# Kernel tuning notes

Measured on AMD Instinct MI355X. Metric: run time of the kernel, lower is better.

## Reference

```python
import jax, jax.numpy as jnp
import numpy as np

N_NODES = 50000
N_EDGES = 600000
IC, H, OC = 64, 128, 32
EPS = 1e-5


def setup_inputs() -> dict:
    key = jax.random.key(0)
    ks = jax.random.split(key, 8)
    x = jax.random.normal(ks[0], (N_NODES, IC), dtype=jnp.float32)
    ei = jax.random.randint(ks[1], (2, N_EDGES), 0, N_NODES, dtype=jnp.int64)
    proj_w = jax.random.normal(ks[2], (IC, H), dtype=jnp.float32) * 0.05
    proj_b = jnp.zeros((H,), dtype=jnp.float32)
    # conv_w[layer, lin, :, :] with lin order: key, query, value, skip
    conv_w = jax.random.normal(ks[3], (3, 4, H, H), dtype=jnp.float32) * 0.05
    conv_b = jnp.zeros((3, 4, H), dtype=jnp.float32)
    bn_gamma = jnp.ones((3, H), dtype=jnp.float32)
    bn_beta = jnp.zeros((3, H), dtype=jnp.float32)
    head_w = jax.random.normal(ks[4], (H, OC), dtype=jnp.float32) * 0.05
    head_b = jnp.zeros((OC,), dtype=jnp.float32)
    return {"x": x, "ei": ei, "proj_w": proj_w, "proj_b": proj_b,
            "conv_w": conv_w, "conv_b": conv_b, "bn_gamma": bn_gamma,
            "bn_beta": bn_beta, "head_w": head_w, "head_b": head_b}


def _res_gated_conv(x, src, dst, w, b):
    # PyG ResGatedGraphConv: out_i = skip(x_i) + sum_j sigmoid(key(x_i)+query(x_j)) * value(x_j)
    k = x @ w[0] + b[0]      # key   (applied to target/dst)
    q = x @ w[1] + b[1]      # query (applied to source/src)
    v = x @ w[2] + b[2]      # value (applied to source/src)
    msg = jax.nn.sigmoid(k[dst] + q[src]) * v[src]          # [E, H]
    agg = jax.ops.segment_sum(msg, dst, num_segments=x.shape[0])  # [N, H]
    return x @ w[3] + b[3] + agg


def _batchnorm(x, gamma, beta):
    # training-mode BatchNorm1d: batch statistics over the node dimension
    mean = jnp.mean(x, axis=0)
    var = jnp.var(x, axis=0)
    return gamma * (x - mean) * jax.lax.rsqrt(var + EPS) + beta


def reference(x, ei, proj_w, proj_b, conv_w, conv_b, bn_gamma, bn_beta, head_w, head_b):
    src, dst = ei[0], ei[1]
    h = jax.nn.relu(x @ proj_w + proj_b)
    for layer in range(3):
        h = _res_gated_conv(h, src, dst, conv_w[layer], conv_b[layer])
        h = jax.nn.relu(_batchnorm(h, bn_gamma[layer], bn_beta[layer]))
        # dropout(p=0.2) is identity in eval mode
    return h @ head_w + head_b
```

## Files before the change

kernel.cpp:

```cpp
#include <hip/hip_runtime.h>
#include <hip/hip_bf16.h>
#include <math.h>

#define HDIM 128
#define ICDIM 64
#define OCDIM 32
#define BN_EPS 1e-5f
#define NCH 64

typedef __attribute__((ext_vector_type(8))) short bv8;
typedef __attribute__((ext_vector_type(4))) float fv4;

static __device__ __forceinline__ unsigned short f2bf(float v) {
    __hip_bfloat16 t = __float2bfloat16(v);
    return *(unsigned short*)&t;
}
static __device__ __forceinline__ float bflo(unsigned int u) {
    union { unsigned int i; float f; } c; c.i = u << 16; return c.f;
}
static __device__ __forceinline__ float bfhi(unsigned int u) {
    union { unsigned int i; float f; } c; c.i = u & 0xffff0000u; return c.f;
}

__global__ void proj_kernel(const float* __restrict__ x,
                            const float* __restrict__ w,
                            const float* __restrict__ b,
                            __hip_bfloat16* __restrict__ h, int n) {
    __shared__ float xs[2][ICDIM];
    int tid = threadIdx.x;
    if (tid < 2 * ICDIM) {
        int r = tid / ICDIM, c = tid % ICDIM;
        int node = blockIdx.x * 2 + r;
        xs[r][c] = (node < n) ? x[(size_t)node * ICDIM + c] : 0.f;
    }
    __syncthreads();
    int node = blockIdx.x * 2 + (tid >> 7);
    if (node >= n) return;
    int c = tid & 127;
    const float* xr = xs[tid >> 7];
    float acc = b[c];
#pragma unroll
    for (int k = 0; k < ICDIM; ++k)
        acc = fmaf(xr[k], w[k * HDIM + c], acc);
    h[(size_t)node * HDIM + c] = __float2bfloat16(fmaxf(acc, 0.f));
}

__global__ void wconv_kernel(const float* __restrict__ src,
                             __hip_bfloat16* __restrict__ dst) {
    int mat = blockIdx.x;
    const float* s = src + (size_t)mat * HDIM * HDIM;
    __hip_bfloat16* d = dst + (size_t)mat * HDIM * HDIM;
    for (int idx = threadIdx.x; idx < HDIM * HDIM; idx += 256) {
        int i = idx >> 7, o = idx & 127;
        d[(size_t)o * HDIM + i] = __float2bfloat16(s[idx]);
    }
}

__global__ __launch_bounds__(1024)
void gemm4_fused_kernel(const __hip_bfloat16* __restrict__ hB,
                        const __hip_bfloat16* __restrict__ wt4,
                        const float* __restrict__ b4,
                        __hip_bfloat16* __restrict__ K,
                        __hip_bfloat16* __restrict__ Q,
                        __hip_bfloat16* __restrict__ V,
                        float* __restrict__ S, int n) {
    __shared__ unsigned short hs[NCH * HDIM];
    const unsigned short* h = (const unsigned short*)hB;
    int tid = threadIdx.x;
    int m0 = blockIdx.x * NCH;

    {
        const uint4* src = (const uint4*)(h + (size_t)m0 * HDIM);
        ((uint4*)hs)[tid] = src[tid];
    }

    int wv = tid >> 6;
    int lane = tid & 63;
    int lin = wv >> 2;
    int g2 = wv & 3;
    int j = lane & 15;
    int kg = lane >> 4;

    const unsigned short* wbase =
        (const unsigned short*)(wt4 + (size_t)lin * HDIM * HDIM);
    bv8 af[2][4];
#pragma unroll
    for (int gs = 0; gs < 2; ++gs)
#pragma unroll
        for (int ks = 0; ks < 4; ++ks)
            af[gs][ks] = *(const bv8*)(wbase +
                (size_t)(g2 * 32 + gs * 16 + j) * HDIM + ks * 32 + kg * 8);

    const float* bl = b4 + lin * HDIM;
    float4 bias0 = *(const float4*)(bl + g2 * 32 + kg * 4);
    float4 bias1 = *(const float4*)(bl + g2 * 32 + 16 + kg * 4);

    __hip_bfloat16* obf = (lin == 0) ? K : (lin == 1) ? Q : V;

    __syncthreads();

#pragma unroll
    for (int t4 = 0; t4 < NCH / 16; ++t4) {
        const unsigned short* hrow = hs + (t4 * 16 + j) * HDIM + kg * 8;
        fv4 acc0 = (fv4){0.f, 0.f, 0.f, 0.f};
        fv4 acc1 = (fv4){0.f, 0.f, 0.f, 0.f};
#pragma unroll
        for (int ks = 0; ks < 4; ++ks) {
            bv8 bf = *(const bv8*)(hrow + ks * 32);
            acc0 = __builtin_amdgcn_mfma_f32_16x16x32_bf16(af[0][ks], bf, acc0, 0, 0, 0);
            acc1 = __builtin_amdgcn_mfma_f32_16x16x32_bf16(af[1][ks], bf, acc1, 0, 0, 0);
        }
        int node = m0 + t4 * 16 + j;
        if (node < n) {
            if (lin == 3) {
                float* o = S + (size_t)node * HDIM + g2 * 32 + kg * 4;
                float4 r0, r1;
                r0.x = acc0.x + bias0.x; r0.y = acc0.y + bias0.y;
                r0.z = acc0.z + bias0.z; r0.w = acc0.w + bias0.w;
                r1.x = acc1.x + bias1.x; r1.y = acc1.y + bias1.y;
                r1.z = acc1.z + bias1.z; r1.w = acc1.w + bias1.w;
                *(float4*)o = r0;
                *(float4*)(o + 16) = r1;
            } else {
                unsigned short* o =
                    (unsigned short*)obf + (size_t)node * HDIM + g2 * 32 + kg * 4;
                ushort4 r0, r1;
                r0.x = f2bf(acc0.x + bias0.x); r0.y = f2bf(acc0.y + bias0.y);
                r0.z = f2bf(acc0.z + bias0.z); r0.w = f2bf(acc0.w + bias0.w);
                r1.x = f2bf(acc1.x + bias1.x); r1.y = f2bf(acc1.y + bias1.y);
                r1.z = f2bf(acc1.z + bias1.z); r1.w = f2bf(acc1.w + bias1.w);
                *(ushort4*)o = r0;
                *(ushort4*)(o + 16) = r1;
            }
        }
    }
}

__global__ void hist_kernel(const int* __restrict__ ei, int* __restrict__ deg, int e) {
    int i = blockIdx.x * 256 + threadIdx.x;
    if (i < e) atomicAdd(&deg[ei[(size_t)e + i]], 1);
}

__global__ void scan1_kernel(const int* __restrict__ deg, int* __restrict__ incl,
                             int* __restrict__ bsum, int n) {
    __shared__ int tmp[256];
    int i = blockIdx.x * 256 + threadIdx.x;
    int v = (i < n) ? deg[i] : 0;
    tmp[threadIdx.x] = v;
    __syncthreads();
    for (int ofs = 1; ofs < 256; ofs <<= 1) {
        int t = (threadIdx.x >= ofs) ? tmp[threadIdx.x - ofs] : 0;
        __syncthreads();
        tmp[threadIdx.x] += t;
        __syncthreads();
    }
    if (i < n) incl[i] = tmp[threadIdx.x];
    if (threadIdx.x == 255) bsum[blockIdx.x] = tmp[255];
}

__global__ void scan2_kernel(int* __restrict__ bsum, int nb) {
    __shared__ int tmp[256];
    int v = (threadIdx.x < nb) ? bsum[threadIdx.x] : 0;
    tmp[threadIdx.x] = v;
    __syncthreads();
    for (int ofs = 1; ofs < 256; ofs <<= 1) {
        int t = (threadIdx.x >= ofs) ? tmp[threadIdx.x - ofs] : 0;
        __syncthreads();
        tmp[threadIdx.x] += t;
        __syncthreads();
    }
    if (threadIdx.x < nb) bsum[threadIdx.x] = tmp[threadIdx.x] - v;
}

__global__ void scan3_kernel(const int* __restrict__ deg, const int* __restrict__ incl,
                             const int* __restrict__ bsum, int* __restrict__ off,
                             int* __restrict__ cursor, int n, int e) {
    int i = blockIdx.x * 256 + threadIdx.x;
    if (i < n) {
        int ex = incl[i] - deg[i] + bsum[blockIdx.x];
        off[i] = ex;
        cursor[i] = ex;
        if (i == n - 1) off[n] = e;
    }
}

__global__ void scatter_kernel(const int* __restrict__ ei, int* __restrict__ cursor,
                               int* __restrict__ esrc, int e) {
    int i = blockIdx.x * 256 + threadIdx.x;
    if (i < e) {
        int dst = ei[(size_t)e + i];
        int pos = atomicAdd(&cursor[dst], 1);
        esrc[pos] = ei[i];
    }
}

__global__ void agg_kernel(const int* __restrict__ off, const int* __restrict__ esrc,
                           const __hip_bfloat16* __restrict__ kb,
                           const __hip_bfloat16* __restrict__ qb,
                           const __hip_bfloat16* __restrict__ vb,
                           float* __restrict__ S, int n) {
    int d = blockIdx.x * 4 + (threadIdx.x >> 6);
    if (d >= n) return;
    int lane = threadIdx.x & 63;
    const unsigned int* qw = (const unsigned int*)qb;
    const unsigned int* vw = (const unsigned int*)vb;
    unsigned int kwu = ((const unsigned int*)kb)[(size_t)d * 64 + lane];
    float k0 = bflo(kwu), k1 = bfhi(kwu);
    float a0 = 0.f, a1 = 0.f;

#define EDGE(qu, vu)                                          \
    {                                                         \
        float g0 = k0 + bflo(qu), g1 = k1 + bfhi(qu);         \
        float e0 = __expf(-g0), e1 = __expf(-g1);             \
        a0 += __fdividef(bflo(vu), 1.f + e0);                 \
        a1 += __fdividef(bfhi(vu), 1.f + e1);                 \
    }

    int j = off[d], s1 = off[d + 1];
    for (; j + 4 <= s1; j += 4) {
        int sA = esrc[j], sB = esrc[j + 1], sC = esrc[j + 2], sD = esrc[j + 3];
        unsigned int qA = qw[(size_t)sA * 64 + lane], vA = vw[(size_t)sA * 64 + lane];
        unsigned int qB = qw[(size_t)sB * 64 + lane], vB = vw[(size_t)sB * 64 + lane];
        unsigned int qC = qw[(size_t)sC * 64 + lane], vC = vw[(size_t)sC * 64 + lane];
        unsigned int qD = qw[(size_t)sD * 64 + lane], vD = vw[(size_t)sD * 64 + lane];
        EDGE(qA, vA); EDGE(qB, vB); EDGE(qC, vC); EDGE(qD, vD);
    }
    for (; j < s1; ++j) {
        int s = esrc[j];
        unsigned int qu = qw[(size_t)s * 64 + lane], vu = vw[(size_t)s * 64 + lane];
        EDGE(qu, vu);
    }
#undef EDGE

    float2* sp = (float2*)(S + (size_t)d * HDIM) + lane;
    float2 old = *sp;
    old.x += a0; old.y += a1;
    *sp = old;
}

__global__ void stats_kernel(const float* __restrict__ s,
                             float* __restrict__ stats, int n) {
    int c = threadIdx.x & 127, rh = threadIdx.x >> 7;
    int r0 = blockIdx.x * 128;
    int r1 = min(r0 + 128, n);
    float sum = 0.f, sq = 0.f;
    for (int r = r0 + rh; r < r1; r += 2) {
        float v = s[(size_t)r * HDIM + c];
        sum += v;
        sq = fmaf(v, v, sq);
    }
    __shared__ float ls[2][HDIM], lq[2][HDIM];
    ls[rh][c] = sum;
    lq[rh][c] = sq;
    __syncthreads();
    if (rh == 0) {
        atomicAdd(&stats[c], ls[0][c] + ls[1][c]);
        atomicAdd(&stats[HDIM + c], lq[0][c] + lq[1][c]);
    }
}

__global__ void bn_relu_kernel(const float* __restrict__ s,
                               const float* __restrict__ stats,
                               const float* __restrict__ gamma,
                               const float* __restrict__ beta,
                               __hip_bfloat16* __restrict__ out, int n) {
    size_t idx = (size_t)blockIdx.x * 256 + threadIdx.x;
    size_t total = (size_t)n * HDIM;
    if (idx >= total) return;
    int c = (int)(idx & 127);
    float invn = 1.f / (float)n;
    float mean = stats[c] * invn;
    float var = stats[HDIM + c] * invn - mean * mean;
    float sc = gamma[c] * rsqrtf(var + BN_EPS);
    float sh = beta[c] - mean * sc;
    float v = fmaf(s[idx], sc, sh);
    out[idx] = __float2bfloat16(fmaxf(v, 0.f));
}

__global__ void head_kernel(const __hip_bfloat16* __restrict__ h,
                            const float* __restrict__ w,
                            const float* __restrict__ b,
                            float* __restrict__ out, int n) {
    __shared__ float hsm[8][HDIM];
    for (int i = threadIdx.x; i < 8 * HDIM; i += 256) {
        int r = i >> 7, c = i & 127;
        int node = blockIdx.x * 8 + r;
        hsm[r][c] = (node < n) ? __bfloat162float(h[(size_t)node * HDIM + c]) : 0.f;
    }
    __syncthreads();
    int c = threadIdx.x & 31;
    int ng = threadIdx.x >> 5;
    int node = blockIdx.x * 8 + ng;
    if (node >= n) return;
    float acc = b[c];
#pragma unroll
    for (int k = 0; k < HDIM; ++k)
        acc = fmaf(hsm[ng][k], w[k * OCDIM + c], acc);
    out[(size_t)node * OCDIM + c] = acc;
}

extern "C" void kernel_launch(void* const* d_in, const int* in_sizes, int n_in,
                              void* d_out, int out_size, void* d_ws, size_t ws_size,
                              hipStream_t stream) {
    const float* x      = (const float*)d_in[0];
    const int*   ei     = (const int*)  d_in[1];
    const float* proj_w = (const float*)d_in[2];
    const float* proj_b = (const float*)d_in[3];
    const float* conv_w = (const float*)d_in[4];
    const float* conv_b = (const float*)d_in[5];
    const float* bn_g   = (const float*)d_in[6];
    const float* bn_b   = (const float*)d_in[7];
    const float* head_w = (const float*)d_in[8];
    const float* head_b = (const float*)d_in[9];
    float* out = (float*)d_out;

    int n = in_sizes[0] / ICDIM;
    int e = in_sizes[1] / 2;

    size_t nh = (size_t)n * HDIM;
    size_t need = nh * 4 + 768 * 4 + 4 * nh * 2 + (size_t)12 * HDIM * HDIM * 2
                + ((size_t)3 * n + (n + 1) + 256 + e) * 4;
    if (ws_size < need) return;

    float* S  = (float*)d_ws;
    float* st = S + nh;
    __hip_bfloat16* h = (__hip_bfloat16*)(st + 768);
    __hip_bfloat16* K = h + nh;
    __hip_bfloat16* Q = K + nh;
    __hip_bfloat16* V = Q + nh;
    __hip_bfloat16* Wt = V + nh;

    int* deg    = (int*)(Wt + (size_t)12 * HDIM * HDIM);
    int* incl   = deg + n;
    int* off    = incl + n;
    int* cursor = off + n + 1;
    int* bsum   = cursor + n;
    int* esrc   = bsum + 256;

    hipMemsetAsync(st, 0, 768 * sizeof(float), stream);
    hipMemsetAsync(deg, 0, (size_t)n * sizeof(int), stream);

    int gb_e = (e + 255) / 256;
    int gb_n = (n + 255) / 256;

    proj_kernel<<<(n + 1) / 2, 256, 0, stream>>>(x, proj_w, proj_b, h, n);
    wconv_kernel<<<12, 256, 0, stream>>>(conv_w, Wt);

    hist_kernel<<<gb_e, 256, 0, stream>>>(ei, deg, e);
    scan1_kernel<<<gb_n, 256, 0, stream>>>(deg, incl, bsum, n);
    scan2_kernel<<<1, 256, 0, stream>>>(bsum, gb_n);
    scan3_kernel<<<gb_n, 256, 0, stream>>>(deg, incl, bsum, off, cursor, n, e);
    scatter_kernel<<<gb_e, 256, 0, stream>>>(ei, cursor, esrc, e);

    int gm = (n + NCH - 1) / NCH;
    for (int l = 0; l < 3; ++l) {
        gemm4_fused_kernel<<<gm, 1024, 0, stream>>>(
            h, Wt + (size_t)l * 4 * HDIM * HDIM, conv_b + (size_t)l * 4 * HDIM,
            K, Q, V, S, n);
        agg_kernel<<<(n + 3) / 4, 256, 0, stream>>>(off, esrc, K, Q, V, S, n);
        stats_kernel<<<(n + 127) / 128, 256, 0, stream>>>(S, st + l * 256, n);
        bn_relu_kernel<<<(int)((nh + 255) / 256), 256, 0, stream>>>(
            S, st + l * 256, bn_g + l * HDIM, bn_b + l * HDIM, h, n);
    }

    head_kernel<<<(n + 7) / 8, 256, 0, stream>>>(h, head_w, head_b, out, n);
}
```

Measured before the change: 537.0 us.

## Use MFMA bf16 for input projection and unroll edge aggregation by eight

Replaces the scalar FMA input-projection kernel with an MFMA bf16 kernel that stages 64-node tiles of x into shared memory as bf16 and uses a pre-transposed bf16 copy of proj_w. It also widens the aggregation loop's unroll from 4 to 8 edges and adds a 2-edge tail. The aim is to cut projection compute time and expose more memory-level parallelism in the gather. It adds a small weight-conversion kernel and rounds x to bf16 before the projection.

```diff
diff --git a/kernel.cpp b/kernel.cpp
--- a/kernel.cpp
+++ b/kernel.cpp
@@ -21,28 +21,8 @@
 static __device__ __forceinline__ float bfhi(unsigned int u) {
     union { unsigned int i; float f; } c; c.i = u & 0xffff0000u; return c.f;
 }
-
-__global__ void proj_kernel(const float* __restrict__ x,
-                            const float* __restrict__ w,
-                            const float* __restrict__ b,
-                            __hip_bfloat16* __restrict__ h, int n) {
-    __shared__ float xs[2][ICDIM];
-    int tid = threadIdx.x;
-    if (tid < 2 * ICDIM) {
-        int r = tid / ICDIM, c = tid % ICDIM;
-        int node = blockIdx.x * 2 + r;
-        xs[r][c] = (node < n) ? x[(size_t)node * ICDIM + c] : 0.f;
-    }
-    __syncthreads();
-    int node = blockIdx.x * 2 + (tid >> 7);
-    if (node >= n) return;
-    int c = tid & 127;
-    const float* xr = xs[tid >> 7];
-    float acc = b[c];
-#pragma unroll
-    for (int k = 0; k < ICDIM; ++k)
-        acc = fmaf(xr[k], w[k * HDIM + c], acc);
-    h[(size_t)node * HDIM + c] = __float2bfloat16(fmaxf(acc, 0.f));
+static __device__ __forceinline__ unsigned int pack2bf(float a, float b) {
+    return (unsigned int)f2bf(a) | ((unsigned int)f2bf(b) << 16);
 }
 
 __global__ void wconv_kernel(const float* __restrict__ src,
@@ -53,6 +33,79 @@
     for (int idx = threadIdx.x; idx < HDIM * HDIM; idx += 256) {
         int i = idx >> 7, o = idx & 127;
         d[(size_t)o * HDIM + i] = __float2bfloat16(s[idx]);
+    }
+}
+
+__global__ void wpconv_kernel(const float* __restrict__ src,
+                              __hip_bfloat16* __restrict__ dst) {
+    for (int idx = threadIdx.x; idx < ICDIM * HDIM; idx += 256) {
+        int i = idx >> 7, o = idx & 127;
+        dst[(size_t)o * ICDIM + i] = __float2bfloat16(src[idx]);
+    }
+}
+
+__global__ __launch_bounds__(256)
+void proj_mfma_kernel(const float* __restrict__ x,
+                      const __hip_bfloat16* __restrict__ wp,
+                      const float* __restrict__ b,
+                      __hip_bfloat16* __restrict__ h, int n) {
+    __shared__ unsigned int xs[NCH * ICDIM / 2];
+    int tid = threadIdx.x;
+    int m0 = blockIdx.x * NCH;
+
+    const float2* xsrc = (const float2*)(x + (size_t)m0 * ICDIM);
+    for (int i = tid; i < NCH * ICDIM / 2; i += 256) {
+        int node = m0 + (i >> 5);
+        float2 v = (node < n) ? xsrc[i] : (float2){0.f, 0.f};
+        xs[i] = pack2bf(v.x, v.y);
+    }
+
+    int wv = tid >> 6;
+    int lane = tid & 63;
+    int j = lane & 15;
+    int kg = lane >> 4;
+
+    bv8 af[2][2];
+#pragma unroll
+    for (int gs = 0; gs < 2; ++gs)
+#pragma unroll
+        for (int ks = 0; ks < 2; ++ks)
+            af[gs][ks] = *(const bv8*)((const unsigned short*)wp +
+                (size_t)(wv * 32 + gs * 16 + j) * ICDIM + ks * 32 + kg * 8);
+
+    float4 bias0 = *(const float4*)(b + wv * 32 + kg * 4);
+    float4 bias1 = *(const float4*)(b + wv * 32 + 16 + kg * 4);
+
+    __syncthreads();
+
+#pragma unroll
+    for (int t4 = 0; t4 < NCH / 16; ++t4) {
+        const unsigned short* xrow =
+            (const unsigned short*)xs + (t4 * 16 + j) * ICDIM + kg * 8;
+        fv4 acc0 = (fv4){0.f, 0.f, 0.f, 0.f};
+        fv4 acc1 = (fv4){0.f, 0.f, 0.f, 0.f};
+#pragma unroll
+        for (int ks = 0; ks < 2; ++ks) {
+            bv8 bf = *(const bv8*)(xrow + ks * 32);
+            acc0 = __builtin_amdgcn_mfma_f32_16x16x32_bf16(af[0][ks], bf, acc0, 0, 0, 0);
+            acc1 = __builtin_amdgcn_mfma_f32_16x16x32_bf16(af[1][ks], bf, acc1, 0, 0, 0);
+        }
+        int node = m0 + t4 * 16 + j;
+        if (node < n) {
+            unsigned short* o =
+                (unsigned short*)h + (size_t)node * HDIM + wv * 32 + kg * 4;
+            ushort4 r0, r1;
+            r0.x = f2bf(fmaxf(acc0.x + bias0.x, 0.f));
+            r0.y = f2bf(fmaxf(acc0.y + bias0.y, 0.f));
+            r0.z = f2bf(fmaxf(acc0.z + bias0.z, 0.f));
+            r0.w = f2bf(fmaxf(acc0.w + bias0.w, 0.f));
+            r1.x = f2bf(fmaxf(acc1.x + bias1.x, 0.f));
+            r1.y = f2bf(fmaxf(acc1.y + bias1.y, 0.f));
+            r1.z = f2bf(fmaxf(acc1.z + bias1.z, 0.f));
+            r1.w = f2bf(fmaxf(acc1.w + bias1.w, 0.f));
+            *(ushort4*)o = r0;
+            *(ushort4*)(o + 16) = r1;
+        }
     }
 }
 
@@ -217,13 +270,25 @@
     }
 
     int j = off[d], s1 = off[d + 1];
-    for (; j + 4 <= s1; j += 4) {
-        int sA = esrc[j], sB = esrc[j + 1], sC = esrc[j + 2], sD = esrc[j + 3];
+    for (; j + 8 <= s1; j += 8) {
+        int sA = esrc[j],     sB = esrc[j + 1], sC = esrc[j + 2], sD = esrc[j + 3];
+        int sE = esrc[j + 4], sF = esrc[j + 5], sG = esrc[j + 6], sH = esrc[j + 7];
         unsigned int qA = qw[(size_t)sA * 64 + lane], vA = vw[(size_t)sA * 64 + lane];
         unsigned int qB = qw[(size_t)sB * 64 + lane], vB = vw[(size_t)sB * 64 + lane];
         unsigned int qC = qw[(size_t)sC * 64 + lane], vC = vw[(size_t)sC * 64 + lane];
         unsigned int qD = qw[(size_t)sD * 64 + lane], vD = vw[(size_t)sD * 64 + lane];
+        unsigned int qE = qw[(size_t)sE * 64 + lane], vE = vw[(size_t)sE * 64 + lane];
+        unsigned int qF = qw[(size_t)sF * 64 + lane], vF = vw[(size_t)sF * 64 + lane];
+        unsigned int qG = qw[(size_t)sG * 64 + lane], vG = vw[(size_t)sG * 64 + lane];
+        unsigned int qH = qw[(size_t)sH * 64 + lane], vH = vw[(size_t)sH * 64 + lane];
         EDGE(qA, vA); EDGE(qB, vB); EDGE(qC, vC); EDGE(qD, vD);
+        EDGE(qE, vE); EDGE(qF, vF); EDGE(qG, vG); EDGE(qH, vH);
+    }
+    for (; j + 2 <= s1; j += 2) {
+        int sA = esrc[j], sB = esrc[j + 1];
+        unsigned int qA = qw[(size_t)sA * 64 + lane], vA = vw[(size_t)sA * 64 + lane];
+        unsigned int qB = qw[(size_t)sB * 64 + lane], vB = vw[(size_t)sB * 64 + lane];
+        EDGE(qA, vA); EDGE(qB, vB);
     }
     for (; j < s1; ++j) {
         int s = esrc[j];
@@ -318,7 +383,8 @@
     int e = in_sizes[1] / 2;
 
     size_t nh = (size_t)n * HDIM;
-    size_t need = nh * 4 + 768 * 4 + 4 * nh * 2 + (size_t)12 * HDIM * HDIM * 2
+    size_t need = nh * 4 + 768 * 4 + 4 * nh * 2
+                + (size_t)12 * HDIM * HDIM * 2 + (size_t)HDIM * ICDIM * 2
                 + ((size_t)3 * n + (n + 1) + 256 + e) * 4;
     if (ws_size < need) return;
 
@@ -329,8 +395,9 @@
     __hip_bfloat16* Q = K + nh;
     __hip_bfloat16* V = Q + nh;
     __hip_bfloat16* Wt = V + nh;
-
-    int* deg    = (int*)(Wt + (size_t)12 * HDIM * HDIM);
+    __hip_bfloat16* Wp = Wt + (size_t)12 * HDIM * HDIM;
+
+    int* deg    = (int*)(Wp + (size_t)HDIM * ICDIM);
     int* incl   = deg + n;
     int* off    = incl + n;
     int* cursor = off + n + 1;
@@ -343,8 +410,9 @@
     int gb_e = (e + 255) / 256;
     int gb_n = (n + 255) / 256;
 
-    proj_kernel<<<(n + 1) / 2, 256, 0, stream>>>(x, proj_w, proj_b, h, n);
     wconv_kernel<<<12, 256, 0, stream>>>(conv_w, Wt);
+    wpconv_kernel<<<1, 256, 0, stream>>>(proj_w, Wp);
+    proj_mfma_kernel<<<(n + NCH - 1) / NCH, 256, 0, stream>>>(x, Wp, proj_b, h, n);
 
     hist_kernel<<<gb_e, 256, 0, stream>>>(ei, deg, e);
     scan1_kernel<<<gb_n, 256, 0, stream>>>(deg, incl, bsum, n);
```

Result: no change. 531.8 us (-1.0%).
